# Kernel optimization log

Measured on AMD Instinct MI355X. Metric: run time of the kernel, lower is better.

The kernel has to match this reference:

```python
import jax, jax.numpy as jnp
import numpy as np

B, L, D = 64, 4096, 1024
FILL = -10000.0  # sentinel used by the original masked_fill before the sort


def setup_inputs() -> dict:
    key = jax.random.key(0)
    k1, k2 = jax.random.split(key)
    features = jax.random.normal(k1, (B, L, D), dtype=jnp.float32)
    lengths = jax.random.randint(k2, (B,), 0, L, dtype=jnp.int32)
    return {"features": features, "lengths": lengths}


def reference(features, lengths):
    # Original: mask invalid positions with -10000, sort descending along seq,
    # zero out masked slots, take element 0. Mathematically this is a masked
    # max over valid positions (and 0 if a sequence has length 0, since the
    # second masked_fill zeroes position 0 when mask[:,0] is False).
    L_ = features.shape[1]
    mask = jnp.arange(L_)[None, :] < lengths[:, None]            # [B, L]
    masked = jnp.where(mask[:, :, None], features, FILL)          # [B, L, D]
    pooled = jnp.max(masked, axis=1)                              # [B, D]
    pooled = jnp.where((lengths > 0)[:, None], pooled, 0.0)
    pool_weights = None
    return pooled
```

## Files before the change

### kernel.cpp

```cpp
#include <hip/hip_runtime.h>

#define FILLV (-10000.0f)

typedef __attribute__((ext_vector_type(4))) float f32x4;

__device__ __forceinline__ f32x4 vmax4(f32x4 a, f32x4 b) {
    f32x4 r;
    r.x = fmaxf(a.x, b.x);
    r.y = fmaxf(a.y, b.y);
    r.z = fmaxf(a.z, b.z);
    r.w = fmaxf(a.w, b.w);
    return r;
}

__device__ __forceinline__ f32x4 ntload(const f32x4* p) {
    return __builtin_nontemporal_load(p);
}

__device__ __forceinline__ f32x4 fillv4() {
    f32x4 v = {FILLV, FILLV, FILLV, FILLV};
    return v;
}

__global__ __launch_bounds__(256, 4)
void feasel_partial_kernel(const float* __restrict__ feat,
                           const int* __restrict__ lengths,
                           float* __restrict__ part,
                           int B, int L, int DV, int seg, int S) {
    __shared__ int off[1025];
    const int t = threadIdx.x;

    for (int b = t; b < B; b += blockDim.x) {
        int len = lengths[b];
        len = len < 0 ? 0 : (len > L ? L : len);
        int n = (len + seg - 1) / seg;
        if (n > S) n = S;
        off[b + 1] = n;
    }
    __syncthreads();
    if (t == 0) {
        off[0] = 0;
        for (int b = 0; b < B; ++b) off[b + 1] += off[b];
    }
    __syncthreads();
    const int W = off[B];

    for (int i = blockIdx.x; i < W; i += gridDim.x) {
        int lo = 0, hi = B;
        while (hi - lo > 1) {
            int m = (lo + hi) >> 1;
            if (off[m] <= i) lo = m; else hi = m;
        }
        const int b = lo;
        const int s = i - off[lo];

        int len = lengths[b];
        len = len > L ? L : len;
        const int l0 = s * seg;
        const int l1 = min(l0 + seg, len);

        const f32x4* __restrict__ p =
            reinterpret_cast<const f32x4*>(feat) + (size_t)b * L * DV + (size_t)l0 * DV + t;

        f32x4 a0 = fillv4(), a1 = fillv4(), a2 = fillv4(), a3 = fillv4();

        int l = l0;
        for (; l + 8 <= l1; l += 8) {
            f32x4 v0 = ntload(p + 0 * (size_t)DV);
            f32x4 v1 = ntload(p + 1 * (size_t)DV);
            f32x4 v2 = ntload(p + 2 * (size_t)DV);
            f32x4 v3 = ntload(p + 3 * (size_t)DV);
            f32x4 v4 = ntload(p + 4 * (size_t)DV);
            f32x4 v5 = ntload(p + 5 * (size_t)DV);
            f32x4 v6 = ntload(p + 6 * (size_t)DV);
            f32x4 v7 = ntload(p + 7 * (size_t)DV);
            a0 = vmax4(a0, vmax4(v0, v4));
            a1 = vmax4(a1, vmax4(v1, v5));
            a2 = vmax4(a2, vmax4(v2, v6));
            a3 = vmax4(a3, vmax4(v3, v7));
            p += 8 * (size_t)DV;
        }
        for (; l < l1; ++l) {
            a0 = vmax4(a0, ntload(p));
            p += DV;
        }
        a0 = vmax4(vmax4(a0, a1), vmax4(a2, a3));

        reinterpret_cast<f32x4*>(part)[((size_t)b * S + s) * DV + t] = a0;
    }
}

__global__ void feasel_reduce_kernel(const float* __restrict__ part,
                                     const int* __restrict__ lengths,
                                     float* __restrict__ out,
                                     int L, int DV, int seg, int S) {
    const int b = blockIdx.x;
    const int c = blockIdx.y * 64 + threadIdx.x;
    if (c >= DV) return;

    int len = lengths[b];
    len = len < 0 ? 0 : (len > L ? L : len);
    int nseg = (len + seg - 1) / seg;
    if (nseg > S) nseg = S;

    f32x4 acc;
    if (len <= 0) {
        f32x4 z = {0.f, 0.f, 0.f, 0.f};
        acc = z;
    } else {
        const f32x4* __restrict__ p =
            reinterpret_cast<const f32x4*>(part) + (size_t)b * S * DV + c;
        f32x4 a0 = fillv4(), a1 = fillv4(), a2 = fillv4(), a3 = fillv4();
        int s = 0;
        for (; s + 4 <= nseg; s += 4) {
            a0 = vmax4(a0, p[(size_t)(s + 0) * DV]);
            a1 = vmax4(a1, p[(size_t)(s + 1) * DV]);
            a2 = vmax4(a2, p[(size_t)(s + 2) * DV]);
            a3 = vmax4(a3, p[(size_t)(s + 3) * DV]);
        }
        for (; s < nseg; ++s)
            a0 = vmax4(a0, p[(size_t)s * DV]);
        acc = vmax4(vmax4(a0, a1), vmax4(a2, a3));
    }
    reinterpret_cast<f32x4*>(out)[(size_t)b * DV + c] = acc;
}

__global__ void feasel_direct_kernel(const float* __restrict__ feat,
                                     const int* __restrict__ lengths,
                                     float* __restrict__ out,
                                     int L, int DV) {
    const int b = blockIdx.x;
    const int t = threadIdx.x;
    int len = lengths[b];
    len = len < 0 ? 0 : (len > L ? L : len);

    const f32x4* __restrict__ p =
        reinterpret_cast<const f32x4*>(feat) + (size_t)b * L * DV + t;

    f32x4 a0 = fillv4(), a1 = fillv4(), a2 = fillv4(), a3 = fillv4();
    int l = 0;
    for (; l + 4 <= len; l += 4) {
        a0 = vmax4(a0, ntload(p + 0 * (size_t)DV));
        a1 = vmax4(a1, ntload(p + 1 * (size_t)DV));
        a2 = vmax4(a2, ntload(p + 2 * (size_t)DV));
        a3 = vmax4(a3, ntload(p + 3 * (size_t)DV));
        p += 4 * (size_t)DV;
    }
    for (; l < len; ++l) {
        a0 = vmax4(a0, ntload(p));
        p += DV;
    }
    a0 = vmax4(vmax4(a0, a1), vmax4(a2, a3));
    if (len <= 0) {
        f32x4 z = {0.f, 0.f, 0.f, 0.f};
        a0 = z;
    }
    reinterpret_cast<f32x4*>(out)[(size_t)b * DV + t] = a0;
}

extern "C" void kernel_launch(void* const* d_in, const int* in_sizes, int n_in,
                              void* d_out, int out_size, void* d_ws, size_t ws_size,
                              hipStream_t stream) {
    const float* feat    = (const float*)d_in[0];
    const int*   lengths = (const int*)d_in[1];
    float*       out     = (float*)d_out;

    const int B  = in_sizes[1];
    const int D  = out_size / B;
    const int DV = D / 4;
    const int L  = in_sizes[0] / (B * D);

    int S = 128;
    while (S > 1 && (size_t)B * S * D * sizeof(float) > ws_size) S >>= 1;

    if ((size_t)B * S * D * sizeof(float) <= ws_size && B <= 1024) {
        float* part   = (float*)d_ws;
        const int seg = (L + S - 1) / S;

        feasel_partial_kernel<<<1024, 256, 0, stream>>>(feat, lengths, part,
                                                        B, L, DV, seg, S);

        dim3 grid2(B, (DV + 63) / 64);
        feasel_reduce_kernel<<<grid2, 64, 0, stream>>>(part, lengths, out, L, DV, seg, S);
    } else {
        feasel_direct_kernel<<<B, DV, 0, stream>>>(feat, lengths, out, L, DV);
    }
}
```

Measured before the change: 105.5 us.

## Replace two-pass partial-segment reduction with atomicMax on order-preserving encoded floats

The per-segment partial buffer and the separate reduce kernel are removed. Each work item now folds its segment max straight into a B×D accumulator using unsigned atomicMax on an order-preserving encoding of the float. A small init kernel and a decode kernel handle setup and the final conversion, including the zero for empty sequences. The segment length drops to a fixed 16 rows, which gives many more work items; this avoids writing and re-reading the partial buffer, but adds heavy atomic traffic and contention on each output address, plus two extra launches.

Result: slower. 169.7 us (+60.9%).

```diff
diff --git a/kernel.cpp b/kernel.cpp
--- a/kernel.cpp
+++ b/kernel.cpp
@@ -22,20 +22,32 @@
     return v;
 }
 
+__device__ __forceinline__ unsigned enc_f32(float f) {
+    unsigned x = __float_as_uint(f);
+    return (x & 0x80000000u) ? ~x : (x | 0x80000000u);
+}
+__device__ __forceinline__ float dec_f32(unsigned u) {
+    unsigned x = (u & 0x80000000u) ? (u ^ 0x80000000u) : ~u;
+    return __uint_as_float(x);
+}
+
+__global__ void feasel_init_kernel(unsigned* __restrict__ acc, int n) {
+    int i = blockIdx.x * blockDim.x + threadIdx.x;
+    if (i < n) acc[i] = enc_f32(FILLV);
+}
+
 __global__ __launch_bounds__(256, 4)
-void feasel_partial_kernel(const float* __restrict__ feat,
-                           const int* __restrict__ lengths,
-                           float* __restrict__ part,
-                           int B, int L, int DV, int seg, int S) {
+void feasel_main_kernel(const float* __restrict__ feat,
+                        const int* __restrict__ lengths,
+                        unsigned* __restrict__ acc,
+                        int B, int L, int DV, int seg) {
     __shared__ int off[1025];
     const int t = threadIdx.x;
 
     for (int b = t; b < B; b += blockDim.x) {
         int len = lengths[b];
         len = len < 0 ? 0 : (len > L ? L : len);
-        int n = (len + seg - 1) / seg;
-        if (n > S) n = S;
-        off[b + 1] = n;
+        off[b + 1] = (len + seg - 1) / seg;
     }
     __syncthreads();
     if (t == 0) {
@@ -86,43 +98,24 @@
         }
         a0 = vmax4(vmax4(a0, a1), vmax4(a2, a3));
 
-        reinterpret_cast<f32x4*>(part)[((size_t)b * S + s) * DV + t] = a0;
+        unsigned* dst = acc + ((size_t)b * DV + t) * 4;
+        atomicMax(dst + 0, enc_f32(a0.x));
+        atomicMax(dst + 1, enc_f32(a0.y));
+        atomicMax(dst + 2, enc_f32(a0.z));
+        atomicMax(dst + 3, enc_f32(a0.w));
     }
 }
 
-__global__ void feasel_reduce_kernel(const float* __restrict__ part,
+__global__ void feasel_decode_kernel(const unsigned* __restrict__ acc,
                                      const int* __restrict__ lengths,
                                      float* __restrict__ out,
-                                     int L, int DV, int seg, int S) {
-    const int b = blockIdx.x;
-    const int c = blockIdx.y * 64 + threadIdx.x;
-    if (c >= DV) return;
-
-    int len = lengths[b];
-    len = len < 0 ? 0 : (len > L ? L : len);
-    int nseg = (len + seg - 1) / seg;
-    if (nseg > S) nseg = S;
-
-    f32x4 acc;
-    if (len <= 0) {
-        f32x4 z = {0.f, 0.f, 0.f, 0.f};
-        acc = z;
-    } else {
-        const f32x4* __restrict__ p =
-            reinterpret_cast<const f32x4*>(part) + (size_t)b * S * DV + c;
-        f32x4 a0 = fillv4(), a1 = fillv4(), a2 = fillv4(), a3 = fillv4();
-        int s = 0;
-        for (; s + 4 <= nseg; s += 4) {
-            a0 = vmax4(a0, p[(size_t)(s + 0) * DV]);
-            a1 = vmax4(a1, p[(size_t)(s + 1) * DV]);
-            a2 = vmax4(a2, p[(size_t)(s + 2) * DV]);
-            a3 = vmax4(a3, p[(size_t)(s + 3) * DV]);
-        }
-        for (; s < nseg; ++s)
-            a0 = vmax4(a0, p[(size_t)s * DV]);
-        acc = vmax4(vmax4(a0, a1), vmax4(a2, a3));
-    }
-    reinterpret_cast<f32x4*>(out)[(size_t)b * DV + c] = acc;
+                                     int D, int n) {
+    int i = blockIdx.x * blockDim.x + threadIdx.x;
+    if (i >= n) return;
+    const int b = i / D;
+    float f = dec_f32(acc[i]);
+    if (lengths[b] <= 0) f = 0.f;
+    out[i] = f;
 }
 
 __global__ void feasel_direct_kernel(const float* __restrict__ feat,
@@ -169,19 +162,18 @@
     const int D  = out_size / B;
     const int DV = D / 4;
     const int L  = in_sizes[0] / (B * D);
+    const int N  = B * D;
 
-    int S = 128;
-    while (S > 1 && (size_t)B * S * D * sizeof(float) > ws_size) S >>= 1;
+    if ((size_t)N * sizeof(unsigned) <= ws_size && B <= 1024) {
+        unsigned* acc = (unsigned*)d_ws;
+        const int seg = 16;
 
-    if ((size_t)B * S * D * sizeof(float) <= ws_size && B <= 1024) {
-        float* part   = (float*)d_ws;
-        const int seg = (L + S - 1) / S;
+        feasel_init_kernel<<<(N + 255) / 256, 256, 0, stream>>>(acc, N);
 
-        feasel_partial_kernel<<<1024, 256, 0, stream>>>(feat, lengths, part,
-                                                        B, L, DV, seg, S);
+        feasel_main_kernel<<<1024, 256, 0, stream>>>(feat, lengths, acc,
+                                                     B, L, DV, seg);
 
-        dim3 grid2(B, (DV + 63) / 64);
-        feasel_reduce_kernel<<<grid2, 64, 0, stream>>>(part, lengths, out, L, DV, seg, S);
+        feasel_decode_kernel<<<(N + 255) / 256, 256, 0, stream>>>(acc, lengths, out, D, N);
     } else {
         feasel_direct_kernel<<<B, DV, 0, stream>>>(feat, lengths, out, L, DV);
     }
```
